# Kernel optimization log

Hardware: AMD Instinct MI355X
Metric: run time of the kernel (lower is better)

The kernel has to match this reference:

```python
import jax, jax.numpy as jnp
import numpy as np

N_NODES = 100000
N_EDGES = 1600000
D_IN = 128
D_OUT = 128
EPSILON = 0.0


def setup_inputs() -> dict:
    key = jax.random.key(0)
    k1, k2, k3, k4, k5 = jax.random.split(key, 5)
    indices = jax.random.randint(k1, (2, N_EDGES), 0, N_NODES, dtype=jnp.int64 if jax.config.jax_enable_x64 else jnp.int32)
    values = jax.random.uniform(k2, (N_EDGES,), dtype=jnp.float32)
    features = jax.random.normal(k3, (N_NODES, D_IN), dtype=jnp.float32)
    # Xavier-uniform linear weights, zero biases (as in init_parameters)
    lim1 = float(np.sqrt(6.0 / (D_IN + D_OUT)))
    lim2 = float(np.sqrt(6.0 / (D_OUT + D_OUT)))
    W1 = jax.random.uniform(k4, (D_IN, D_OUT), minval=-lim1, maxval=lim1, dtype=jnp.float32)
    W2 = jax.random.uniform(k5, (D_OUT, D_OUT), minval=-lim2, maxval=lim2, dtype=jnp.float32)
    b1 = jnp.zeros((D_OUT,), dtype=jnp.float32)
    b2 = jnp.zeros((D_OUT,), dtype=jnp.float32)
    return {"indices": indices, "values": values, "features": features,
            "W1": W1, "b1": b1, "W2": W2, "b2": b2}


def reference(indices, values, features, W1, b1, W2, b2):
    row, col = indices[0], indices[1]
    # SpMM: out[r] = sum_e values[e] * features[col[e]]  (sparse_adj @ features)
    messages = values[:, None] * features[col]              # [E, D_IN]
    neighbor = jax.ops.segment_sum(messages, row, num_segments=N_NODES)  # [N, D_IN]
    combined = (1.0 + EPSILON) * features + neighbor        # epsilon residual
    h = jax.nn.relu(combined @ W1 + b1)                     # Linear -> ReLU
    out = h @ W2 + b2                                       # Linear
    # dropout is identity in eval mode
    return out
```

## Files before the change

### kernel.cpp

```cpp
#include <hip/hip_runtime.h>

#define N_NODES 100000
#define N_EDGES 1600000
#define D 128
#define CB 98
#define CCAP 17920

typedef unsigned short u16;
typedef unsigned int u32;
typedef __attribute__((ext_vector_type(8))) short bf16x8;
typedef __attribute__((ext_vector_type(4))) float f32x4;

__device__ __forceinline__ u16 f2bf(float f) {
    u32 u = __float_as_uint(f);
    u += 0x7fffu + ((u >> 16) & 1u);
    return (u16)(u >> 16);
}


#define BIN_BLKS 391
#define CF_BLKS 6250
#define CW_BLKS 128

__global__ __launch_bounds__(256) void prep(
    const float* __restrict__ features, u32* __restrict__ featb,
    const float* __restrict__ W1, const float* __restrict__ W2,
    u16* __restrict__ W1t, u16* __restrict__ W2t,
    const int* __restrict__ row, const int* __restrict__ col,
    const float* __restrict__ val,
    int* __restrict__ coarseCount, int2* __restrict__ binned) {
    __shared__ int h[CB];
    __shared__ int lb[CB];
    int bid = blockIdx.x;
    int t = threadIdx.x;

    if (bid >= BIN_BLKS) {
        int cid = bid - BIN_BLKS;
        if (cid < CF_BLKS) {
            int idx = cid * 256 + t;
            const float4* f4 = (const float4*)features;
            float4 a = f4[idx * 2], b = f4[idx * 2 + 1];
            uint4 o;
            o.x = (u32)f2bf(a.x) | ((u32)f2bf(a.y) << 16);
            o.y = (u32)f2bf(a.z) | ((u32)f2bf(a.w) << 16);
            o.z = (u32)f2bf(b.x) | ((u32)f2bf(b.y) << 16);
            o.w = (u32)f2bf(b.z) | ((u32)f2bf(b.w) << 16);
            ((uint4*)featb)[idx] = o;
        } else {
            int flat = (cid - CF_BLKS) * 256 + t;
            int m = flat >> 14;
            int idx = flat & 16383;
            int n = idx & 127;
            int k = idx >> 7;
            const float* src = m ? W2 : W1;
            u16* dst = m ? W2t : W1t;
            dst[n * 128 + k] = f2bf(src[k * 128 + n]);
        }
        return;
    }

    if (t < CB) h[t] = 0;
    __syncthreads();
    int base = bid * 4096;
    int r[16];
#pragma unroll
    for (int i = 0; i < 16; ++i) {
        int e = base + i * 256 + t;
        r[i] = (e < N_EDGES) ? row[e] : -1;
        if (r[i] >= 0) atomicAdd(&h[r[i] >> 10], 1);
    }
    __syncthreads();
    if (t < CB) {
        int c = h[t];
        lb[t] = c ? atomicAdd(&coarseCount[t * 16], c) : 0;
        h[t] = 0;
    }
    __syncthreads();
#pragma unroll
    for (int i = 0; i < 16; ++i) {
        if (r[i] < 0) continue;
        int e = base + i * 256 + t;
        int cb = r[i] >> 10;
        int pos = cb * CCAP + lb[cb] + atomicAdd(&h[cb], 1);
        int2 ev;
        ev.x = col[e] | ((r[i] & 1023) << 17);
        ev.y = __float_as_int(val[e]);
        binned[pos] = ev;
    }
}


__global__ __launch_bounds__(1024) void sortk(const int2* __restrict__ binned,
                                              const int* __restrict__ coarseCount,
                                              int2* __restrict__ rowRange,
                                              int2* __restrict__ scev) {
    __shared__ int h[1024];
    __shared__ int cur[1024];
    __shared__ int wsum[16];
    __shared__ int wbase[16];
    int b = blockIdx.x, t = threadIdx.x;
    int lane = t & 63, wv = t >> 6;
    int row0 = b << 10;
    int lo = b * CCAP;
    int cnt = coarseCount[b * 16];

    h[t] = 0;
    __syncthreads();
    for (int i = t; i < cnt; i += 1024)
        atomicAdd(&h[((u32)binned[lo + i].x) >> 17], 1);
    __syncthreads();

    int c = h[t];
    int x = c;
#pragma unroll
    for (int d = 1; d < 64; d <<= 1) {
        int y = __shfl_up(x, d);
        if (lane >= d) x += y;
    }
    if (lane == 63) wsum[wv] = x;
    __syncthreads();
    if (t < 16) {
        int s = wsum[t], sx = s;
#pragma unroll
        for (int d = 1; d < 16; d <<= 1) {
            int y = __shfl_up(sx, d);
            if (lane >= d) sx += y;
        }
        wbase[t] = sx - s;
    }
    __syncthreads();
    int start = lo + wbase[wv] + (x - c);
    if (row0 + t < N_NODES) rowRange[row0 + t] = make_int2(start, start + c);
    cur[t] = start;
    __syncthreads();

    for (int i = t; i < cnt; i += 1024) {
        int2 ev = binned[lo + i];
        int rl = ((u32)ev.x) >> 17;
        int pos = atomicAdd(&cur[rl], 1);
        scev[pos] = make_int2(ev.x & 0x1FFFF, ev.y);
    }
}


__global__ __launch_bounds__(256) void spmm_bf16(
    const int2* __restrict__ scev, const int2* __restrict__ rowRange,
    const u32* __restrict__ featb, u32* __restrict__ Xb) {
    int wid0 = (blockIdx.x * blockDim.x + threadIdx.x) >> 6;
    int wid = __builtin_amdgcn_readfirstlane(wid0);
    int lane = threadIdx.x & 63;
    if (wid >= N_NODES) return;
    int2 rr = rowRange[wid];
    int j = rr.x, end = rr.y;
    u32 self = featb[wid * 64 + lane];
    float ax0 = __uint_as_float(self << 16);
    float ay0 = __uint_as_float(self & 0xffff0000u);
    float ax1 = 0.f, ay1 = 0.f;
    for (; j < end; j += 16) {
        int2 e[16];
        u32 p[16];
#pragma unroll
        for (int u = 0; u < 16; ++u) {
            int idx = j + u;
            int c = (idx < end) ? idx : (end - 1);
            e[u] = scev[c];
            if (idx >= end) e[u].y = 0;
        }
#pragma unroll
        for (int u = 0; u < 16; ++u) p[u] = featb[e[u].x * 64 + lane];
#pragma unroll
        for (int u = 0; u < 16; ++u) {
            float v = __int_as_float(e[u].y);
            float lo = __uint_as_float(p[u] << 16);
            float hi = __uint_as_float(p[u] & 0xffff0000u);
            if (u & 1) {
                ax1 += v * lo;
                ay1 += v * hi;
            } else {
                ax0 += v * lo;
                ay0 += v * hi;
            }
        }
    }
    float accx = ax0 + ax1;
    float accy = ay0 + ay1;
    Xb[wid * 64 + lane] = (u32)f2bf(accx) | ((u32)f2bf(accy) << 16);
}


__global__ __launch_bounds__(256, 2) void gemm_fused(
    const u16* __restrict__ Xb, const u16* __restrict__ W1t,
    const float* __restrict__ b1, const u16* __restrict__ W2t,
    const float* __restrict__ b2, float* __restrict__ outf) {
    __shared__ u16 Ws[128][136];
    u16(*Ht)[130] = (u16(*)[130]) & Ws[0][0];

    int t = threadIdx.x;
    {
        const uint4* wsrc = (const uint4*)W1t;
#pragma unroll
        for (int i = 0; i < 8; ++i) {
            int f = t + 256 * i;
            *(uint4*)&Ws[f >> 4][(f & 15) << 3] = wsrc[f];
        }
    }
    __syncthreads();

    int w = t >> 6, lane = t & 63;
    int quad = lane >> 4, l16 = lane & 15;
    int row0 = blockIdx.x * 128 + w * 32;

    f32x4 acc[2][8];
#pragma unroll
    for (int rt = 0; rt < 2; ++rt)
#pragma unroll
        for (int ct = 0; ct < 8; ++ct) acc[rt][ct] = (f32x4){0.f, 0.f, 0.f, 0.f};

    int ra = row0 + l16;
    int rb = row0 + 16 + l16;
    if (ra > N_NODES - 1) ra = N_NODES - 1;
    if (rb > N_NODES - 1) rb = N_NODES - 1;
    const u16* pa = Xb + (size_t)ra * D + quad * 8;
    const u16* pb = Xb + (size_t)rb * D + quad * 8;

#pragma unroll
    for (int kb = 0; kb < 128; kb += 32) {
        bf16x8 a0 = *(const bf16x8*)(pa + kb);
        bf16x8 a1 = *(const bf16x8*)(pb + kb);
#pragma unroll
        for (int ct = 0; ct < 8; ++ct) {
            bf16x8 b = *(const bf16x8*)&Ws[ct * 16 + l16][kb + quad * 8];
            acc[0][ct] = __builtin_amdgcn_mfma_f32_16x16x32_bf16(a0, b, acc[0][ct], 0, 0, 0);
            acc[1][ct] = __builtin_amdgcn_mfma_f32_16x16x32_bf16(a1, b, acc[1][ct], 0, 0, 0);
        }
    }

    float bv1[8];
#pragma unroll
    for (int ct = 0; ct < 8; ++ct) bv1[ct] = b1[ct * 16 + l16];

    __syncthreads();

    int hbase = w * 32;
#pragma unroll
    for (int rt = 0; rt < 2; ++rt) {
#pragma unroll
        for (int ct = 0; ct < 8; ++ct) {
            float v0 = fmaxf(acc[rt][ct][0] + bv1[ct], 0.f);
            float v1 = fmaxf(acc[rt][ct][1] + bv1[ct], 0.f);
            float v2 = fmaxf(acc[rt][ct][2] + bv1[ct], 0.f);
            float v3 = fmaxf(acc[rt][ct][3] + bv1[ct], 0.f);
            u16* dst = &Ht[ct * 16 + l16][hbase + rt * 16 + quad * 4];
            ((u32*)dst)[0] = (u32)f2bf(v0) | ((u32)f2bf(v1) << 16);
            ((u32*)dst)[1] = (u32)f2bf(v2) | ((u32)f2bf(v3) << 16);
        }
    }
    __syncthreads();

    f32x4 acc2[2][8];
#pragma unroll
    for (int rt = 0; rt < 2; ++rt)
#pragma unroll
        for (int ct = 0; ct < 8; ++ct) acc2[rt][ct] = (f32x4){0.f, 0.f, 0.f, 0.f};

#pragma unroll
    for (int kb = 0; kb < 128; kb += 32) {
        bf16x8 a0, a1;
#pragma unroll
        for (int i = 0; i < 8; ++i) {
            a0[i] = (short)Ht[kb + quad * 8 + i][hbase + l16];
            a1[i] = (short)Ht[kb + quad * 8 + i][hbase + 16 + l16];
        }
#pragma unroll
        for (int ct = 0; ct < 8; ++ct) {
            bf16x8 b = *(const bf16x8*)(W2t + (size_t)(ct * 16 + l16) * D + kb + quad * 8);
            acc2[0][ct] = __builtin_amdgcn_mfma_f32_16x16x32_bf16(a0, b, acc2[0][ct], 0, 0, 0);
            acc2[1][ct] = __builtin_amdgcn_mfma_f32_16x16x32_bf16(a1, b, acc2[1][ct], 0, 0, 0);
        }
    }

    float bv2[8];
#pragma unroll
    for (int ct = 0; ct < 8; ++ct) bv2[ct] = b2[ct * 16 + l16];

#pragma unroll
    for (int rt = 0; rt < 2; ++rt) {
#pragma unroll
        for (int r = 0; r < 4; ++r) {
            int row = row0 + rt * 16 + quad * 4 + r;
            if (row >= N_NODES) continue;
#pragma unroll
            for (int ct = 0; ct < 8; ++ct) {
                outf[(size_t)row * D + ct * 16 + l16] = acc2[rt][ct][r] + bv2[ct];
            }
        }
    }
}

extern "C" void kernel_launch(void* const* d_in, const int* in_sizes, int n_in,
                              void* d_out, int out_size, void* d_ws, size_t ws_size,
                              hipStream_t stream) {
    const int* indices = (const int*)d_in[0];
    const float* values = (const float*)d_in[1];
    const float* features = (const float*)d_in[2];
    const float* W1 = (const float*)d_in[3];
    const float* b1 = (const float*)d_in[4];
    const float* W2 = (const float*)d_in[5];
    const float* b2 = (const float*)d_in[6];

    const int* row = indices;
    const int* col = indices + N_EDGES;

    int* wsI = (int*)d_ws;
    int* coarseCount = wsI;
    int2* rowRange = (int2*)(wsI + 1600);
    int2* scev = (int2*)(wsI + 1600 + 2 * N_NODES);
    u32* Xb = (u32*)(wsI + 1600 + 2 * N_NODES + 2 * CB * CCAP);
    u16* W1t = (u16*)(Xb + (size_t)N_NODES * 64);
    u16* W2t = W1t + 16384;

    int2* binned = (int2*)d_out;
    u32* featb = (u32*)((char*)d_out + (size_t)N_NODES * D * 2);
    float* outf = (float*)d_out;

    hipMemsetAsync(coarseCount, 0, CB * 16 * sizeof(int), stream);

    prep<<<BIN_BLKS + CF_BLKS + CW_BLKS, 256, 0, stream>>>(
        features, featb, W1, W2, W1t, W2t, row, col, values, coarseCount, binned);

    sortk<<<CB, 1024, 0, stream>>>(binned, coarseCount, rowRange, scev);

    spmm_bf16<<<(N_NODES * 64 + 255) / 256, 256, 0, stream>>>(scev, rowRange, featb, Xb);

    gemm_fused<<<(N_NODES + 127) / 128, 256, 0, stream>>>(
        (const u16*)Xb, W1t, b1, W2t, b2, outf);
}
```

Baseline: 252.7 us.

## Double-buffer SpMM neighbor gathers via async global-to-LDS loads

The SpMM gather loop now issues each batch of 16 neighbor feature loads with global_load_lds straight into a per-wave LDS staging buffer. Two buffers alternate, and vmcnt waits let one batch be consumed while the next is in flight. The goal is to keep more gather memory traffic outstanding per wave and hide its latency behind the FMA work. In exchange it adds 32KB of LDS per block, which can cut occupancy. It also relies on hand-counted vmcnt values being right, which holds only if the index loads are not counted as vector memory operations.

```diff
diff --git a/kernel.cpp b/kernel.cpp
--- a/kernel.cpp
+++ b/kernel.cpp
@@ -146,9 +146,10 @@
 __global__ __launch_bounds__(256) void spmm_bf16(
     const int2* __restrict__ scev, const int2* __restrict__ rowRange,
     const u32* __restrict__ featb, u32* __restrict__ Xb) {
-    int wid0 = (blockIdx.x * blockDim.x + threadIdx.x) >> 6;
-    int wid = __builtin_amdgcn_readfirstlane(wid0);
-    int lane = threadIdx.x & 63;
+    __shared__ u32 stage[4][2][16][64];
+    int tid = threadIdx.x;
+    int wv = tid >> 6, lane = tid & 63;
+    int wid = __builtin_amdgcn_readfirstlane((blockIdx.x * blockDim.x + tid) >> 6);
     if (wid >= N_NODES) return;
     int2 rr = rowRange[wid];
     int j = rr.x, end = rr.y;
@@ -156,32 +157,68 @@
     float ax0 = __uint_as_float(self << 16);
     float ay0 = __uint_as_float(self & 0xffff0000u);
     float ax1 = 0.f, ay1 = 0.f;
-    for (; j < end; j += 16) {
-        int2 e[16];
-        u32 p[16];
-#pragma unroll
-        for (int u = 0; u < 16; ++u) {
-            int idx = j + u;
-            int c = (idx < end) ? idx : (end - 1);
-            e[u] = scev[c];
-            if (idx >= end) e[u].y = 0;
-        }
-#pragma unroll
-        for (int u = 0; u < 16; ++u) p[u] = featb[e[u].x * 64 + lane];
-#pragma unroll
-        for (int u = 0; u < 16; ++u) {
-            float v = __int_as_float(e[u].y);
-            float lo = __uint_as_float(p[u] << 16);
-            float hi = __uint_as_float(p[u] & 0xffff0000u);
-            if (u & 1) {
-                ax1 += v * lo;
-                ay1 += v * hi;
-            } else {
-                ax0 += v * lo;
-                ay0 += v * hi;
-            }
-        }
-    }
+
+    if (j < end) {
+        u32(*bufA)[64] = stage[wv][0];
+        u32(*bufB)[64] = stage[wv][1];
+        int VA[16], VB[16];
+
+#define LOADG(V, BUF, JB)                                                     \
+    _Pragma("unroll") for (int u = 0; u < 16; ++u) {                          \
+        int idx = (JB) + u;                                                   \
+        int c = (idx < end) ? idx : (end - 1);     \
+        int2 ev = scev[c];                                                    \
+        if (idx >= end) ev.y = 0;            \
+        V[u] = ev.y;                                                          \
+        __builtin_amdgcn_global_load_lds(                                     \
+            (const __attribute__((address_space(1))) u32*)(featb +            \
+                                                           ev.x * 64 + lane), \
+            (__attribute__((address_space(3))) u32*)&BUF[u][0], 4, 0, 0);     \
+    }
+
+#define CONS(V, BUF)                                                          \
+    _Pragma("unroll") for (int u = 0; u < 16; ++u) {                          \
+        float v = __int_as_float(V[u]);                                       \
+        u32 p = BUF[u][lane];                                                 \
+        float lo = __uint_as_float(p << 16);                                  \
+        float hi = __uint_as_float(p & 0xffff0000u);                          \
+        if (u & 1) { ax1 += v * lo; ay1 += v * hi; }                          \
+        else       { ax0 += v * lo; ay0 += v * hi; }                          \
+    }
+
+#define WAIT16 asm volatile("s_waitcnt vmcnt(16)" ::: "memory")
+#define WAIT0 asm volatile("s_waitcnt vmcnt(0)" ::: "memory")
+
+        int nb = (end - j + 15) >> 4;
+        LOADG(VA, bufA, j);
+        int jb = j + 16;
+        int b = 1;
+        while (b + 1 < nb) {
+            LOADG(VB, bufB, jb);
+            WAIT16;
+            CONS(VA, bufA);
+            LOADG(VA, bufA, jb + 16);
+            WAIT16;
+            CONS(VB, bufB);
+            jb += 32;
+            b += 2;
+        }
+        if (b < nb) {
+            LOADG(VB, bufB, jb);
+            WAIT16;
+            CONS(VA, bufA);
+            WAIT0;
+            CONS(VB, bufB);
+        } else {
+            WAIT0;
+            CONS(VA, bufA);
+        }
+#undef LOADG
+#undef CONS
+#undef WAIT16
+#undef WAIT0
+    }
+
     float accx = ax0 + ax1;
     float accy = ay0 + ay1;
     Xb[wid * 64 + lane] = (u32)f2bf(accx) | ((u32)f2bf(accy) << 16);
```

New measurement: 284.1 us. +12.4%, slower.
